# Optimization experiments

Hardware: AMD Instinct MI355X
Metric: run time of the kernel (lower is better)

The kernel has to match this reference:

```python
import jax, jax.numpy as jnp
import numpy as np

B, S, E = 2, 2048, 2048
H, D = 16, 128
I = 8192
EPS = 1e-5


def layernorm(x, w, b):
    mu = jnp.mean(x, axis=-1, keepdims=True)
    var = jnp.mean(jnp.square(x - mu), axis=-1, keepdims=True)
    return (x - mu) * jax.lax.rsqrt(var + EPS) * w + b


def setup_inputs() -> dict:
    key = jax.random.key(0)
    ks = jax.random.split(key, 6)
    s = 0.02
    return {
        "x": jax.random.normal(ks[0], (B, S, E), jnp.float32),
        "ln1_w": jnp.ones((E,), jnp.float32),
        "ln1_b": jnp.zeros((E,), jnp.float32),
        "Wqkv": jax.random.normal(ks[1], (E, 3 * E), jnp.float32) * s,
        "Wo": jax.random.normal(ks[2], (E, E), jnp.float32) * s,
        "ln2_w": jnp.ones((E,), jnp.float32),
        "ln2_b": jnp.zeros((E,), jnp.float32),
        "W1": jax.random.normal(ks[3], (E, I), jnp.float32) * s,
        "W2": jax.random.normal(ks[4], (I, E), jnp.float32) * s,
    }


def reference(x, ln1_w, ln1_b, Wqkv, Wo, ln2_w, ln2_b, W1, W2):
    scale = D ** -0.5
    # --- attention sublayer (pre-LN) ---
    h = layernorm(x, ln1_w, ln1_b)
    qkv = (h @ Wqkv).reshape(B, S, 3, H, D)
    q, k, v = [jnp.moveaxis(qkv[:, :, i], 1, 2) for i in range(3)]  # [B,H,S,D]
    scores = jnp.einsum("bhqd,bhkd->bhqk", q, k) * scale
    causal = jnp.triu(jnp.ones((S, S), bool), k=1)
    scores = jnp.where(causal, -jnp.inf, scores)
    attn = jax.nn.softmax(scores, axis=-1)
    out = jnp.einsum("bhqk,bhkd->bqhd", attn, v).reshape(B, S, E)
    x = x + out @ Wo
    # --- FFN sublayer (pre-LN) ---
    h = layernorm(x, ln2_w, ln2_b)
    x = x + jax.nn.gelu(h @ W1, approximate=True) @ W2
    return x
```

## Files before the change

### kernel.cpp

```cpp
#include <hip/hip_runtime.h>
#include <hip/hip_bf16.h>

#define B_ 2
#define S_ 2048
#define E_ 2048
#define H_ 16
#define D_ 128
#define I_ 8192
#define T_ (B_*S_)

typedef __attribute__((ext_vector_type(8))) short bf16x8;
typedef __attribute__((ext_vector_type(8))) unsigned short us8;
typedef __attribute__((ext_vector_type(4))) float f32x4;

__device__ __forceinline__ unsigned short f2bf(float f) {
  union { float f; unsigned int u; } c; c.f = f;
  unsigned int u = c.u;
  unsigned int r = (u + 0x7fffu + ((u >> 16) & 1u)) >> 16;
  return (unsigned short)r;
}

__device__ __forceinline__ void gload16(const void* g, void* l) {
  __builtin_amdgcn_global_load_lds((const __attribute__((address_space(1))) void*)g,
                                   (__attribute__((address_space(3))) void*)l, 16, 0, 0);
}

__global__ void transpose_w(const float* __restrict__ in, unsigned short* __restrict__ out,
                            int K, int N) {
  __shared__ float tile[32][33];
  const int n0 = blockIdx.x * 32, k0 = blockIdx.y * 32;
  const int tx = threadIdx.x, ty = threadIdx.y;
#pragma unroll
  for (int j = 0; j < 4; ++j) {
    int k = k0 + ty + j * 8;
    tile[ty + j * 8][tx] = in[(size_t)k * N + n0 + tx];
  }
  __syncthreads();
#pragma unroll
  for (int j = 0; j < 4; ++j) {
    int n = n0 + ty + j * 8;
    out[(size_t)n * K + k0 + tx] = f2bf(tile[tx][ty + j * 8]);
  }
}

__global__ void ln_kernel(const float* __restrict__ x, const float* __restrict__ w,
                          const float* __restrict__ b, unsigned short* __restrict__ out) {
  const int row = blockIdx.x;
  const int tid = threadIdx.x;
  const int wid = tid >> 6, lane = tid & 63;
  const float4* xr = (const float4*)(x + (size_t)row * E_);
  float4 v0 = xr[tid * 2], v1 = xr[tid * 2 + 1];
  float s  = v0.x + v0.y + v0.z + v0.w + v1.x + v1.y + v1.z + v1.w;
  float sq = v0.x*v0.x + v0.y*v0.y + v0.z*v0.z + v0.w*v0.w
           + v1.x*v1.x + v1.y*v1.y + v1.z*v1.z + v1.w*v1.w;
#pragma unroll
  for (int off = 32; off > 0; off >>= 1) {
    s  += __shfl_xor(s, off);
    sq += __shfl_xor(sq, off);
  }
  __shared__ float red[8];
  if (lane == 0) { red[wid] = s; red[wid + 4] = sq; }
  __syncthreads();
  s  = red[0] + red[1] + red[2] + red[3];
  sq = red[4] + red[5] + red[6] + red[7];
  const float mu  = s * (1.0f / E_);
  const float var = sq * (1.0f / E_) - mu * mu;
  const float rstd = rsqrtf(var + 1e-5f);
  const float4* w4 = (const float4*)w + tid * 2;
  const float4* b4 = (const float4*)b + tid * 2;
  float4 w0 = w4[0], w1 = w4[1], bb0 = b4[0], bb1 = b4[1];
  us8 o;
  o[0] = f2bf((v0.x - mu) * rstd * w0.x + bb0.x);
  o[1] = f2bf((v0.y - mu) * rstd * w0.y + bb0.y);
  o[2] = f2bf((v0.z - mu) * rstd * w0.z + bb0.z);
  o[3] = f2bf((v0.w - mu) * rstd * w0.w + bb0.w);
  o[4] = f2bf((v1.x - mu) * rstd * w1.x + bb1.x);
  o[5] = f2bf((v1.y - mu) * rstd * w1.y + bb1.y);
  o[6] = f2bf((v1.z - mu) * rstd * w1.z + bb1.z);
  o[7] = f2bf((v1.w - mu) * rstd * w1.w + bb1.w);
  *(us8*)(&out[(size_t)row * E_ + tid * 8]) = o;
}

template<int EPI>
__global__ void gemm_bt(const unsigned short* __restrict__ A,
                        const unsigned short* __restrict__ Bt,
                        void* __restrict__ Cout,
                        const float* __restrict__ resid,
                        int M, int N, int K) {
  __shared__ __align__(16) unsigned short As[128 * 32];
  __shared__ __align__(16) unsigned short Bs[128 * 32];
  const int gn = N >> 7;
  const int nwg = (M >> 7) * gn;
  const int cpx = nwg >> 3;
  const int bid = blockIdx.x;
  const int swz = (bid & 7) * cpx + (bid >> 3);
  const int bm = swz / gn, bn = swz % gn;
  const int tid = threadIdx.x;
  const int wid = tid >> 6, lane = tid & 63;
  const int fr = lane & 15, kg = lane >> 4;
  const int wr = wid >> 1, wc = wid & 1;

  const int c0 = wid * 2;
  const unsigned short* gA = A  + (size_t)(bm * 128 + c0 * 16 + (lane >> 2)) * K + (lane & 3) * 8;
  const unsigned short* gB = Bt + (size_t)(bn * 128 + c0 * 16 + (lane >> 2)) * K + (lane & 3) * 8;
  unsigned short* lA = &As[c0 * 512];
  unsigned short* lB = &Bs[c0 * 512];

  const unsigned short* rA = &As[(wr * 64 + fr) * 32 + kg * 8];
  const unsigned short* rB = &Bs[(wc * 64 + fr) * 32 + kg * 8];

  f32x4 acc[4][4] = {};
  const int nk = K >> 5;
  for (int kt = 0; kt < nk; ++kt) {
    __syncthreads();
    gload16(gA,                 lA);
    gload16(gA + 16 * (size_t)K, lA + 512);
    gload16(gB,                 lB);
    gload16(gB + 16 * (size_t)K, lB + 512);
    gA += 32; gB += 32;
    __syncthreads();
    bf16x8 af[4], bfr[4];
#pragma unroll
    for (int m = 0; m < 4; ++m) af[m]  = *(const bf16x8*)(rA + m * 16 * 32);
#pragma unroll
    for (int n = 0; n < 4; ++n) bfr[n] = *(const bf16x8*)(rB + n * 16 * 32);
#pragma unroll
    for (int m = 0; m < 4; ++m)
#pragma unroll
      for (int n = 0; n < 4; ++n)
        acc[m][n] = __builtin_amdgcn_mfma_f32_16x16x32_bf16(af[m], bfr[n], acc[m][n], 0, 0, 0);
  }

  const int row0 = bm * 128 + wr * 64;
  const int col0 = bn * 128 + wc * 64;
#pragma unroll
  for (int m = 0; m < 4; ++m) {
#pragma unroll
    for (int n = 0; n < 4; ++n) {
#pragma unroll
      for (int r = 0; r < 4; ++r) {
        const int row = row0 + m * 16 + kg * 4 + r;
        const int col = col0 + n * 16 + fr;
        const size_t idx = (size_t)row * N + col;
        const float v = acc[m][n][r];
        if constexpr (EPI == 0) {
          ((unsigned short*)Cout)[idx] = f2bf(v);
        } else if constexpr (EPI == 1) {
          const float u = 0.7978845608028654f * (v + 0.044715f * v * v * v);
          const float gel = 0.5f * v * (1.0f + tanhf(u));
          ((unsigned short*)Cout)[idx] = f2bf(gel);
        } else {
          ((float*)Cout)[idx] = v + resid[idx];
        }
      }
    }
  }
}

__global__ void extract_vT(const unsigned short* __restrict__ qkv, unsigned short* __restrict__ vT) {
  __shared__ unsigned short tile[32][34];
  const int bh = blockIdx.z;
  const int b = bh >> 4, h = bh & 15;
  const int s0 = blockIdx.y * 32, d0 = blockIdx.x * 32;
  const int tx = threadIdx.x, ty = threadIdx.y;
#pragma unroll
  for (int j = 0; j < 4; ++j) {
    int s = s0 + ty + j * 8;
    tile[ty + j * 8][tx] = qkv[(size_t)(b * S_ + s) * 6144 + 4096 + h * 128 + d0 + tx];
  }
  __syncthreads();
#pragma unroll
  for (int j = 0; j < 4; ++j) {
    int d = d0 + ty + j * 8;
    vT[((size_t)bh * 128 + d) * 2048 + s0 + tx] = tile[tx][ty + j * 8];
  }
}

__global__ __launch_bounds__(256, 2)
void attn_kernel(const unsigned short* __restrict__ qkv,
                 const unsigned short* __restrict__ vT,
                 unsigned short* __restrict__ outp) {
  __shared__ __align__(16) unsigned short Ks[64 * 128];
  __shared__ __align__(16) unsigned short Vts[128 * 64];
  __shared__ __align__(16) unsigned short Ps[4 * 16 * 40];
  const int qt = blockIdx.x;
  const int bh = blockIdx.y;
  const int b = bh >> 4, h = bh & 15;
  const int tid = threadIdx.x, wid = tid >> 6, lane = tid & 63;
  const int fr = lane & 15, g = lane >> 4;

  const unsigned short* qptr = qkv + (size_t)(b * S_ + qt * 64 + wid * 16 + fr) * 6144 + h * 128;
  bf16x8 qf[4];
#pragma unroll
  for (int dc = 0; dc < 4; ++dc) qf[dc] = *(const bf16x8*)(qptr + dc * 32 + g * 8);

  float m0[4], l0[4];
#pragma unroll
  for (int r = 0; r < 4; ++r) { m0[r] = -1e30f; l0[r] = 0.0f; }
  f32x4 acc[8] = {};

  const unsigned short* kbase = qkv + (size_t)(b * S_) * 6144 + 2048 + h * 128;
  const unsigned short* vbase = vT + (size_t)bh * 128 * 2048;
  unsigned short* Pw = &Ps[wid * 640];
  const float scale = 0.08838834764831845f;

  us8 kreg[4], vreg[4];
#pragma unroll
  for (int j = 0; j < 4; ++j) {
    const int cc = tid + 256 * j;
    kreg[j] = *(const us8*)(kbase + (size_t)(cc >> 4) * 6144 + (cc & 15) * 8);
    vreg[j] = *(const us8*)(vbase + (size_t)(cc >> 3) * 2048 + (cc & 7) * 8);
  }

  for (int kt = 0; kt <= qt; ++kt) {
    __syncthreads();
#pragma unroll
    for (int j = 0; j < 4; ++j) {
      const int cc = tid + 256 * j;
      const int krow = cc >> 4, kcp = cc & 15;
      *(us8*)(&Ks[krow * 128 + ((kcp * 8) ^ ((krow & 7) << 3))]) = kreg[j];
      const int drow = cc >> 3, vcp = cc & 7;
      *(us8*)(&Vts[drow * 64 + ((vcp * 8) ^ ((drow & 7) << 3))]) = vreg[j];
    }
    if (kt < qt) {
#pragma unroll
      for (int j = 0; j < 4; ++j) {
        const int cc = tid + 256 * j;
        kreg[j] = *(const us8*)(kbase + (size_t)((kt + 1) * 64 + (cc >> 4)) * 6144 + (cc & 15) * 8);
        vreg[j] = *(const us8*)(vbase + (size_t)(cc >> 3) * 2048 + (kt + 1) * 64 + (cc & 7) * 8);
      }
    }
    __syncthreads();

    f32x4 sc[4] = {};
    __builtin_amdgcn_s_setprio(1);
#pragma unroll
    for (int dc = 0; dc < 4; ++dc) {
#pragma unroll
      for (int sub = 0; sub < 4; ++sub) {
        const int row = sub * 16 + fr;
        bf16x8 kf = *(const bf16x8*)(&Ks[row * 128 + ((dc * 32 + g * 8) ^ ((row & 7) << 3))]);
        sc[sub] = __builtin_amdgcn_mfma_f32_16x16x32_bf16(qf[dc], kf, sc[sub], 0, 0, 0);
      }
    }
    __builtin_amdgcn_s_setprio(0);

    float p[4][4];
    const bool diag = (kt == qt);
#pragma unroll
    for (int sub = 0; sub < 4; ++sub) {
#pragma unroll
      for (int r = 0; r < 4; ++r) {
        float v = sc[sub][r] * scale;
        if (diag && (sub * 16 + fr > wid * 16 + g * 4 + r)) v = -1e30f;
        p[sub][r] = v;
      }
    }
    float corr[4];
#pragma unroll
    for (int r = 0; r < 4; ++r) {
      float mx = fmaxf(fmaxf(p[0][r], p[1][r]), fmaxf(p[2][r], p[3][r]));
#pragma unroll
      for (int off = 1; off < 16; off <<= 1) mx = fmaxf(mx, __shfl_xor(mx, off));
      const float mn = fmaxf(m0[r], mx);
      corr[r] = __expf(m0[r] - mn);
      m0[r] = mn;
      float rs = 0.0f;
#pragma unroll
      for (int sub = 0; sub < 4; ++sub) { p[sub][r] = __expf(p[sub][r] - mn); rs += p[sub][r]; }
#pragma unroll
      for (int off = 1; off < 16; off <<= 1) rs += __shfl_xor(rs, off);
      l0[r] = l0[r] * corr[r] + rs;
    }
#pragma unroll
    for (int dt = 0; dt < 8; ++dt)
#pragma unroll
      for (int r = 0; r < 4; ++r) acc[dt][r] *= corr[r];

#pragma unroll
    for (int half = 0; half < 2; ++half) {
#pragma unroll
      for (int s2 = 0; s2 < 2; ++s2)
#pragma unroll
        for (int r = 0; r < 4; ++r)
          Pw[(g * 4 + r) * 40 + s2 * 16 + fr] = f2bf(p[half * 2 + s2][r]);
      bf16x8 pf = *(const bf16x8*)(&Pw[fr * 40 + g * 8]);
      __builtin_amdgcn_s_setprio(1);
#pragma unroll
      for (int dt = 0; dt < 8; ++dt) {
        const int row = dt * 16 + fr;
        bf16x8 vf = *(const bf16x8*)(&Vts[row * 64 + ((half * 32 + g * 8) ^ ((row & 7) << 3))]);
        acc[dt] = __builtin_amdgcn_mfma_f32_16x16x32_bf16(pf, vf, acc[dt], 0, 0, 0);
      }
      __builtin_amdgcn_s_setprio(0);
    }
  }

  float inv[4];
#pragma unroll
  for (int r = 0; r < 4; ++r) inv[r] = 1.0f / l0[r];
#pragma unroll
  for (int dt = 0; dt < 8; ++dt)
#pragma unroll
    for (int r = 0; r < 4; ++r) {
      const size_t row = (size_t)(b * S_ + qt * 64 + wid * 16 + g * 4 + r);
      outp[row * E_ + h * 128 + dt * 16 + fr] = f2bf(acc[dt][r] * inv[r]);
    }
}

extern "C" void kernel_launch(void* const* d_in, const int* in_sizes, int n_in,
                              void* d_out, int out_size, void* d_ws, size_t ws_size,
                              hipStream_t stream) {
  (void)in_sizes; (void)n_in; (void)out_size; (void)ws_size;
  const float* x    = (const float*)d_in[0];
  const float* ln1w = (const float*)d_in[1];
  const float* ln1b = (const float*)d_in[2];
  const float* Wqkv = (const float*)d_in[3];
  const float* Wo   = (const float*)d_in[4];
  const float* ln2w = (const float*)d_in[5];
  const float* ln2b = (const float*)d_in[6];
  const float* W1   = (const float*)d_in[7];
  const float* W2   = (const float*)d_in[8];
  float* out = (float*)d_out;
  char* ws = (char*)d_ws;

  unsigned short* WqkvT = (unsigned short*)(ws + 0);
  unsigned short* WoT   = (unsigned short*)(ws + 25165824);
  unsigned short* W1T   = (unsigned short*)(ws + 33554432);
  unsigned short* W2T   = (unsigned short*)(ws + 67108864);
  unsigned short* qkvb  = (unsigned short*)(ws + 100663296);
  unsigned short* vTb   = (unsigned short*)(ws + 150994944);
  unsigned short* gbuf  = (unsigned short*)(ws + 100663296);
  unsigned short* hbuf  = (unsigned short*)(ws + 167772160);
  float*          x1    = (float*)         (ws + 184549376);

  const dim3 tb(32, 8);
  hipLaunchKernelGGL(transpose_w, dim3(6144 / 32, 2048 / 32), tb, 0, stream, Wqkv, WqkvT, 2048, 6144);
  hipLaunchKernelGGL(transpose_w, dim3(2048 / 32, 2048 / 32), tb, 0, stream, Wo,   WoT,   2048, 2048);
  hipLaunchKernelGGL(transpose_w, dim3(8192 / 32, 2048 / 32), tb, 0, stream, W1,   W1T,   2048, 8192);
  hipLaunchKernelGGL(transpose_w, dim3(2048 / 32, 8192 / 32), tb, 0, stream, W2,   W2T,   8192, 2048);

  hipLaunchKernelGGL(ln_kernel, dim3(T_), dim3(256), 0, stream, x, ln1w, ln1b, hbuf);
  hipLaunchKernelGGL((gemm_bt<0>), dim3(32 * 48), dim3(256), 0, stream,
                     hbuf, WqkvT, (void*)qkvb, (const float*)nullptr, T_, 6144, 2048);
  hipLaunchKernelGGL(extract_vT, dim3(4, 64, 32), tb, 0, stream, qkvb, vTb);
  hipLaunchKernelGGL(attn_kernel, dim3(S_ / 64, B_ * H_), dim3(256), 0, stream, qkvb, vTb, hbuf);
  hipLaunchKernelGGL((gemm_bt<2>), dim3(32 * 16), dim3(256), 0, stream,
                     hbuf, WoT, (void*)x1, x, T_, 2048, 2048);
  hipLaunchKernelGGL(ln_kernel, dim3(T_), dim3(256), 0, stream, x1, ln2w, ln2b, hbuf);
  hipLaunchKernelGGL((gemm_bt<1>), dim3(32 * 64), dim3(256), 0, stream,
                     hbuf, W1T, (void*)gbuf, (const float*)nullptr, T_, 8192, 2048);
  hipLaunchKernelGGL((gemm_bt<2>), dim3(32 * 16), dim3(256), 0, stream,
                     gbuf, W2T, (void*)out, x1, T_, 2048, 8192);
}
```

Baseline: 797.5 us.

## Switch GEMMs to 32x32x16 MFMA with 64-wide K tiles and XOR-swizzled LDS

Rewrites the shared GEMM kernel to use 32x32x16 bf16 MFMA instructions in place of 16x16x32, doubles the K tile per iteration from 32 to 64, and XOR-swizzles the LDS layout for both global-to-LDS loads and fragment reads. The aim is fewer LDS reads per MFMA, fewer barriers per unit of K, and fewer bank conflicts. A launch bound hinting 3 blocks per CU is added. The costs are twice the LDS per block and a different epilogue store pattern, which may change occupancy and store coalescing.

```diff
diff --git a/kernel.cpp b/kernel.cpp
--- a/kernel.cpp
+++ b/kernel.cpp
@@ -12,6 +12,7 @@
 typedef __attribute__((ext_vector_type(8))) short bf16x8;
 typedef __attribute__((ext_vector_type(8))) unsigned short us8;
 typedef __attribute__((ext_vector_type(4))) float f32x4;
+typedef __attribute__((ext_vector_type(16))) float f32x16;
 
 __device__ __forceinline__ unsigned short f2bf(float f) {
   union { float f; unsigned int u; } c; c.f = f;
@@ -82,13 +83,14 @@
 }
 
 template<int EPI>
-__global__ void gemm_bt(const unsigned short* __restrict__ A,
-                        const unsigned short* __restrict__ Bt,
-                        void* __restrict__ Cout,
-                        const float* __restrict__ resid,
-                        int M, int N, int K) {
-  __shared__ __align__(16) unsigned short As[128 * 32];
-  __shared__ __align__(16) unsigned short Bs[128 * 32];
+__global__ __launch_bounds__(256, 3)
+void gemm32(const unsigned short* __restrict__ A,
+            const unsigned short* __restrict__ Bt,
+            void* __restrict__ Cout,
+            const float* __restrict__ resid,
+            int M, int N, int K) {
+  __shared__ __align__(16) unsigned short As[128 * 64];
+  __shared__ __align__(16) unsigned short Bs[128 * 64];
   const int gn = N >> 7;
   const int nwg = (M >> 7) * gn;
   const int cpx = nwg >> 3;
@@ -97,52 +99,61 @@
   const int bm = swz / gn, bn = swz % gn;
   const int tid = threadIdx.x;
   const int wid = tid >> 6, lane = tid & 63;
-  const int fr = lane & 15, kg = lane >> 4;
   const int wr = wid >> 1, wc = wid & 1;
-
-  const int c0 = wid * 2;
-  const unsigned short* gA = A  + (size_t)(bm * 128 + c0 * 16 + (lane >> 2)) * K + (lane & 3) * 8;
-  const unsigned short* gB = Bt + (size_t)(bn * 128 + c0 * 16 + (lane >> 2)) * K + (lane & 3) * 8;
-  unsigned short* lA = &As[c0 * 512];
-  unsigned short* lB = &Bs[c0 * 512];
-
-  const unsigned short* rA = &As[(wr * 64 + fr) * 32 + kg * 8];
-  const unsigned short* rB = &Bs[(wc * 64 + fr) * 32 + kg * 8];
-
-  f32x4 acc[4][4] = {};
-  const int nk = K >> 5;
+  const int r31 = lane & 31, hi = lane >> 5;
+
+  const int c_s   = (tid & 7) ^ ((tid >> 3) & 7);
+  const int row_s = (tid >> 3) * 2 + (c_s >> 2);
+  const int k_s   = (c_s & 3) * 8;
+  const unsigned short* gA = A  + (size_t)(bm * 128 + row_s) * K + k_s;
+  const unsigned short* gB = Bt + (size_t)(bn * 128 + row_s) * K + k_s;
+  unsigned short* lA = &As[tid * 8];
+  unsigned short* lB = &Bs[tid * 8];
+
+  const int pq  = (r31 >> 1) & 7;
+  const int prA = (wr * 32 + (r31 >> 1)) * 64;
+  const int prB = (wc * 32 + (r31 >> 1)) * 64;
+  const int clo = (r31 & 1) * 4 + hi;
+
+  f32x16 acc[2][2] = {};
+  const int nk = K >> 6;
   for (int kt = 0; kt < nk; ++kt) {
     __syncthreads();
-    gload16(gA,                 lA);
-    gload16(gA + 16 * (size_t)K, lA + 512);
-    gload16(gB,                 lB);
-    gload16(gB + 16 * (size_t)K, lB + 512);
-    gA += 32; gB += 32;
+#pragma unroll
+    for (int s = 0; s < 4; ++s) {
+      gload16(gA + (size_t)((s & 1) * 64) * K + (s >> 1) * 32, lA + s * 2048);
+      gload16(gB + (size_t)((s & 1) * 64) * K + (s >> 1) * 32, lB + s * 2048);
+    }
+    gA += 64; gB += 64;
     __syncthreads();
-    bf16x8 af[4], bfr[4];
-#pragma unroll
-    for (int m = 0; m < 4; ++m) af[m]  = *(const bf16x8*)(rA + m * 16 * 32);
-#pragma unroll
-    for (int n = 0; n < 4; ++n) bfr[n] = *(const bf16x8*)(rB + n * 16 * 32);
-#pragma unroll
-    for (int m = 0; m < 4; ++m)
-#pragma unroll
-      for (int n = 0; n < 4; ++n)
-        acc[m][n] = __builtin_amdgcn_mfma_f32_16x16x32_bf16(af[m], bfr[n], acc[m][n], 0, 0, 0);
+#pragma unroll
+    for (int ks = 0; ks < 4; ++ks) {
+      const int kh = (ks >> 1) * 4096;
+      const int pc = ((clo + (ks & 1) * 2) ^ pq) * 8;
+      bf16x8 a0 = *(const bf16x8*)(&As[kh + prA +        pc]);
+      bf16x8 a1 = *(const bf16x8*)(&As[kh + prA + 1024 + pc]);
+      bf16x8 b0 = *(const bf16x8*)(&Bs[kh + prB +        pc]);
+      bf16x8 b1 = *(const bf16x8*)(&Bs[kh + prB + 1024 + pc]);
+      acc[0][0] = __builtin_amdgcn_mfma_f32_32x32x16_bf16(a0, b0, acc[0][0], 0, 0, 0);
+      acc[0][1] = __builtin_amdgcn_mfma_f32_32x32x16_bf16(a0, b1, acc[0][1], 0, 0, 0);
+      acc[1][0] = __builtin_amdgcn_mfma_f32_32x32x16_bf16(a1, b0, acc[1][0], 0, 0, 0);
+      acc[1][1] = __builtin_amdgcn_mfma_f32_32x32x16_bf16(a1, b1, acc[1][1], 0, 0, 0);
+    }
   }
 
   const int row0 = bm * 128 + wr * 64;
   const int col0 = bn * 128 + wc * 64;
 #pragma unroll
-  for (int m = 0; m < 4; ++m) {
-#pragma unroll
-    for (int n = 0; n < 4; ++n) {
-#pragma unroll
-      for (int r = 0; r < 4; ++r) {
-        const int row = row0 + m * 16 + kg * 4 + r;
-        const int col = col0 + n * 16 + fr;
+  for (int mt = 0; mt < 2; ++mt) {
+#pragma unroll
+    for (int nt = 0; nt < 2; ++nt) {
+#pragma unroll
+      for (int rg = 0; rg < 16; ++rg) {
+        const int rl = (rg & 3) + 8 * (rg >> 2) + 4 * hi;
+        const int row = row0 + mt * 32 + rl;
+        const int col = col0 + nt * 32 + r31;
         const size_t idx = (size_t)row * N + col;
-        const float v = acc[m][n][r];
+        const float v = acc[mt][nt][rg];
         if constexpr (EPI == 0) {
           ((unsigned short*)Cout)[idx] = f2bf(v);
         } else if constexpr (EPI == 1) {
@@ -341,15 +352,15 @@
   hipLaunchKernelGGL(transpose_w, dim3(2048 / 32, 8192 / 32), tb, 0, stream, W2,   W2T,   8192, 2048);
 
   hipLaunchKernelGGL(ln_kernel, dim3(T_), dim3(256), 0, stream, x, ln1w, ln1b, hbuf);
-  hipLaunchKernelGGL((gemm_bt<0>), dim3(32 * 48), dim3(256), 0, stream,
+  hipLaunchKernelGGL((gemm32<0>), dim3(32 * 48), dim3(256), 0, stream,
                      hbuf, WqkvT, (void*)qkvb, (const float*)nullptr, T_, 6144, 2048);
   hipLaunchKernelGGL(extract_vT, dim3(4, 64, 32), tb, 0, stream, qkvb, vTb);
   hipLaunchKernelGGL(attn_kernel, dim3(S_ / 64, B_ * H_), dim3(256), 0, stream, qkvb, vTb, hbuf);
-  hipLaunchKernelGGL((gemm_bt<2>), dim3(32 * 16), dim3(256), 0, stream,
+  hipLaunchKernelGGL((gemm32<2>), dim3(32 * 16), dim3(256), 0, stream,
                      hbuf, WoT, (void*)x1, x, T_, 2048, 2048);
   hipLaunchKernelGGL(ln_kernel, dim3(T_), dim3(256), 0, stream, x1, ln2w, ln2b, hbuf);
-  hipLaunchKernelGGL((gemm_bt<1>), dim3(32 * 64), dim3(256), 0, stream,
+  hipLaunchKernelGGL((gemm32<1>), dim3(32 * 64), dim3(256), 0, stream,
                      hbuf, W1T, (void*)gbuf, (const float*)nullptr, T_, 8192, 2048);
-  hipLaunchKernelGGL((gemm_bt<2>), dim3(32 * 16), dim3(256), 0, stream,
+  hipLaunchKernelGGL((gemm32<2>), dim3(32 * 16), dim3(256), 0, stream,
                      gbuf, W2T, (void*)out, x1, T_, 2048, 8192);
 }
```

Measured after the change: 799.3 us. Within noise of the previous version (+0.2%).
